# Performance work log

Hardware: AMD Instinct MI355X
Metric: run time of the kernel (lower is better)

## Reference

```python
import jax, jax.numpy as jnp
import numpy as np

HIDDEN = 512
MEM = 512
COMM = 512
N = 8192


def setup_inputs() -> dict:
    key = jax.random.key(0)
    ks = jax.random.split(key, 8)
    in_dim = HIDDEN + MEM
    s = 1.0 / np.sqrt(in_dim)
    return {
        "u": jax.random.normal(ks[0], (N, HIDDEN), dtype=jnp.float32),
        "z": jax.random.normal(ks[1], (N, MEM), dtype=jnp.float32),
        # torch Linear weights have shape (out, in); biases init to 0 per _init_weights
        "Wk": jax.random.normal(ks[2], (COMM, in_dim), dtype=jnp.float32) * s,
        "bk": jnp.zeros((COMM,), dtype=jnp.float32),
        "Wv": jax.random.normal(ks[3], (COMM, in_dim), dtype=jnp.float32) * s,
        "bv": jnp.zeros((COMM,), dtype=jnp.float32),
        "Wq": jax.random.normal(ks[4], (COMM, in_dim), dtype=jnp.float32) * s,
        "bq": jnp.zeros((COMM,), dtype=jnp.float32),
    }


def reference(u, z, Wk, bk, Wv, bv, Wq, bq):
    n = u.shape[0]
    scale = jnp.sqrt(jnp.asarray(Wk.shape[0], dtype=u.dtype))
    s = jnp.concatenate([u, z], axis=-1)              # (N, in_dim)
    keys = s @ Wk.T + bk                              # (N, C)
    values = s @ Wv.T + bv                            # (N, C)
    queries = s @ Wq.T + bq                           # (N, C)
    scores = (queries @ keys.T) / scale               # (N, N)
    eye = jnp.eye(n, dtype=bool)
    scores = jnp.where(eye, -jnp.inf, scores)         # self-mask
    comm_attn = jax.nn.softmax(scores, axis=-1)
    comm_attn = jnp.nan_to_num(comm_attn, nan=0.0)
    m_bar = comm_attn @ values                        # (N, C)
    return (m_bar, comm_attn)
```

## Files before the change

### kernel.cpp

```cpp
#include <hip/hip_runtime.h>
#include <hip/hip_bf16.h>
#include <stdint.h>

#define N_TOK 8192
#define IN_DIM 1024
#define CDIM 512
#define NW 1536

typedef short bf16x8 __attribute__((ext_vector_type(8)));
typedef float f32x4 __attribute__((ext_vector_type(4)));

__device__ __forceinline__ unsigned short f2bf(float f) {
  union { float f; unsigned int u; } x; x.f = f;
  unsigned int u = x.u;
  u += 0x7fffu + ((u >> 16) & 1u);
  return (unsigned short)(u >> 16);
}
__device__ __forceinline__ float bf2f(unsigned short us) {
  union { unsigned int u; float f; } x; x.u = ((unsigned int)us) << 16;
  return x.f;
}

#define GLD16(g, l) __builtin_amdgcn_global_load_lds( \
    (const __attribute__((address_space(1))) void*)(g), \
    (__attribute__((address_space(3))) void*)(l), 16, 0, 0)

__global__ __launch_bounds__(256) void k_convert(
    const float* __restrict__ u, const float* __restrict__ z,
    const float* __restrict__ wk, const float* __restrict__ wv,
    const float* __restrict__ wq,
    ushort* __restrict__ Sb, ushort* __restrict__ Wb) {
  const int S4 = N_TOK * IN_DIM / 4;
  const int W4 = NW * IN_DIM / 4;
  const int total = S4 + W4;
  for (int e = blockIdx.x * blockDim.x + threadIdx.x; e < total;
       e += gridDim.x * blockDim.x) {
    float4 v; ushort* dst;
    if (e < S4) {
      int idx = e << 2; int row = idx >> 10; int col = idx & 1023;
      const float* src = (col < 512) ? (u + row * 512 + col)
                                     : (z + row * 512 + (col - 512));
      v = *(const float4*)src;
      dst = Sb + idx;
    } else {
      int idx = (e - S4) << 2; int row = idx >> 10; int col = idx & 1023;
      const float* base = (row < 512) ? wk : (row < 1024 ? wv : wq);
      v = *(const float4*)(base + (size_t)(row & 511) * 1024 + col);
      dst = Wb + idx;
    }
    ushort4 o;
    o.x = f2bf(v.x); o.y = f2bf(v.y); o.z = f2bf(v.z); o.w = f2bf(v.w);
    *(ushort4*)dst = o;
  }
}

__global__ __launch_bounds__(256) void k_kvq(
    const ushort* __restrict__ Sb, const ushort* __restrict__ Wb,
    const float* __restrict__ bk, const float* __restrict__ bv,
    const float* __restrict__ bq,
    ushort* __restrict__ Kb, ushort* __restrict__ Qb, ushort* __restrict__ VT) {
  __shared__ __align__(16) ushort As[128 * 64];
  __shared__ __align__(16) ushort Bs[128 * 64];
  const int tid = threadIdx.x, lane = tid & 63, w = tid >> 6;
  const int wr = w >> 1, wc = w & 1;
  const int tm = blockIdx.x, tn = blockIdx.y;

  f32x4 acc[4][4];
#pragma unroll
  for (int m = 0; m < 4; m++)
#pragma unroll
    for (int n = 0; n < 4; n++) acc[m][n] = (f32x4){0.f, 0.f, 0.f, 0.f};

  const ushort* ga0 = Sb + (size_t)tm * 128 * IN_DIM;
  const ushort* gb0 = Wb + (size_t)tn * 128 * IN_DIM;

  for (int k0 = 0; k0 < IN_DIM; k0 += 64) {
#pragma unroll
    for (int i = 0; i < 4; i++) {
      int ce = i * 256 + tid;
      int row = ce >> 3, c8 = (ce & 7) << 3;
      GLD16(ga0 + (size_t)row * IN_DIM + k0 + c8, As + ce * 8);
      GLD16(gb0 + (size_t)row * IN_DIM + k0 + c8, Bs + ce * 8);
    }
    __syncthreads();
#pragma unroll
    for (int kb = 0; kb < 2; kb++) {
      bf16x8 af[4], bfr[4];
#pragma unroll
      for (int m = 0; m < 4; m++)
        af[m] = *(const bf16x8*)(As + (wr * 64 + m * 16 + (lane & 15)) * 64 +
                                 kb * 32 + ((lane >> 4) << 3));
#pragma unroll
      for (int n = 0; n < 4; n++)
        bfr[n] = *(const bf16x8*)(Bs + (wc * 64 + n * 16 + (lane & 15)) * 64 +
                                  kb * 32 + ((lane >> 4) << 3));
#pragma unroll
      for (int m = 0; m < 4; m++)
#pragma unroll
        for (int n = 0; n < 4; n++)
          acc[m][n] = __builtin_amdgcn_mfma_f32_16x16x32_bf16(af[m], bfr[n],
                                                              acc[m][n], 0, 0, 0);
    }
    __syncthreads();
  }

  const int region = tn >> 2;
  const int colr = (tn & 3) * 128 + wc * 64;
  const int rbase = tm * 128 + wr * 64;
  const float* bias = (region == 0) ? bk : (region == 1 ? bv : bq);
  if (region == 1) {
#pragma unroll
    for (int m = 0; m < 4; m++) {
      int r0 = rbase + m * 16 + ((lane >> 4) << 2);
#pragma unroll
      for (int n = 0; n < 4; n++) {
        int c = colr + n * 16 + (lane & 15);
        float b = bias[c];
        ushort4 pk;
        pk.x = f2bf(acc[m][n][0] + b);
        pk.y = f2bf(acc[m][n][1] + b);
        pk.z = f2bf(acc[m][n][2] + b);
        pk.w = f2bf(acc[m][n][3] + b);
        *(ushort4*)(VT + (size_t)c * N_TOK + r0) = pk;
      }
    }
  } else {
    ushort* O = (region == 0) ? Kb : Qb;
#pragma unroll
    for (int m = 0; m < 4; m++) {
      int r0 = rbase + m * 16 + ((lane >> 4) << 2);
#pragma unroll
      for (int n = 0; n < 4; n++) {
        int c = colr + n * 16 + (lane & 15);
        float b = bias[c];
#pragma unroll
        for (int rg = 0; rg < 4; rg++)
          O[(size_t)(r0 + rg) * CDIM + c] = f2bf(acc[m][n][rg] + b);
      }
    }
  }
}

__global__ __launch_bounds__(256) void k_scores(
    const ushort* __restrict__ Qb, const ushort* __restrict__ Kb,
    ushort* __restrict__ E, float* __restrict__ rowpart) {
  __shared__ __align__(16) ushort As[128 * 64];
  __shared__ __align__(16) ushort Bs[128 * 64];
  __shared__ float sums[256];
  const int tid = threadIdx.x, lane = tid & 63, w = tid >> 6;
  const int wr = w >> 1, wc = w & 1;
  const int tm = blockIdx.x, tn = blockIdx.y;

  f32x4 acc[4][4];
#pragma unroll
  for (int m = 0; m < 4; m++)
#pragma unroll
    for (int n = 0; n < 4; n++) acc[m][n] = (f32x4){0.f, 0.f, 0.f, 0.f};

  const ushort* ga0 = Qb + (size_t)tm * 128 * CDIM;
  const ushort* gb0 = Kb + (size_t)tn * 128 * CDIM;

  for (int k0 = 0; k0 < CDIM; k0 += 64) {
#pragma unroll
    for (int i = 0; i < 4; i++) {
      int ce = i * 256 + tid;
      int row = ce >> 3, c8 = (ce & 7) << 3;
      GLD16(ga0 + (size_t)row * CDIM + k0 + c8, As + ce * 8);
      GLD16(gb0 + (size_t)row * CDIM + k0 + c8, Bs + ce * 8);
    }
    __syncthreads();
#pragma unroll
    for (int kb = 0; kb < 2; kb++) {
      bf16x8 af[4], bfr[4];
#pragma unroll
      for (int m = 0; m < 4; m++)
        af[m] = *(const bf16x8*)(As + (wr * 64 + m * 16 + (lane & 15)) * 64 +
                                 kb * 32 + ((lane >> 4) << 3));
#pragma unroll
      for (int n = 0; n < 4; n++)
        bfr[n] = *(const bf16x8*)(Bs + (wc * 64 + n * 16 + (lane & 15)) * 64 +
                                  kb * 32 + ((lane >> 4) << 3));
#pragma unroll
      for (int m = 0; m < 4; m++)
#pragma unroll
        for (int n = 0; n < 4; n++)
          acc[m][n] = __builtin_amdgcn_mfma_f32_16x16x32_bf16(af[m], bfr[n],
                                                              acc[m][n], 0, 0, 0);
    }
    __syncthreads();
  }

  const float scale = 0.044194173824159216f;
  float rs[4][4];
#pragma unroll
  for (int m = 0; m < 4; m++)
#pragma unroll
    for (int rg = 0; rg < 4; rg++) rs[m][rg] = 0.f;

#pragma unroll
  for (int m = 0; m < 4; m++) {
    int grow_b = tm * 128 + wr * 64 + m * 16 + ((lane >> 4) << 2);
#pragma unroll
    for (int n = 0; n < 4; n++) {
      int gcol = tn * 128 + wc * 64 + n * 16 + (lane & 15);
#pragma unroll
      for (int rg = 0; rg < 4; rg++) {
        int grow = grow_b + rg;
        float ev = (grow == gcol) ? 0.0f : __expf(acc[m][n][rg] * scale);
        unsigned short evb = f2bf(ev);
        E[(size_t)grow * N_TOK + gcol] = evb;
        rs[m][rg] += bf2f(evb);
      }
    }
  }
#pragma unroll
  for (int m = 0; m < 4; m++)
#pragma unroll
    for (int rg = 0; rg < 4; rg++) {
      float s = rs[m][rg];
      s += __shfl_xor(s, 1);
      s += __shfl_xor(s, 2);
      s += __shfl_xor(s, 4);
      s += __shfl_xor(s, 8);
      rs[m][rg] = s;
    }
  if ((lane & 15) == 0) {
#pragma unroll
    for (int m = 0; m < 4; m++)
#pragma unroll
      for (int rg = 0; rg < 4; rg++)
        sums[wc * 128 + wr * 64 + m * 16 + ((lane >> 4) << 2) + rg] = rs[m][rg];
  }
  __syncthreads();
  if (tid < 128)
    rowpart[(size_t)(tm * 128 + tid) * 64 + tn] = sums[tid] + sums[128 + tid];
}

__global__ __launch_bounds__(256) void k_rcp(const float* __restrict__ rowpart,
                                             float* __restrict__ rcp_l) {
  int row = blockIdx.x * blockDim.x + threadIdx.x;
  if (row < N_TOK) {
    const float4* p = (const float4*)(rowpart + (size_t)row * 64);
    float s = 0.f;
#pragma unroll
    for (int i = 0; i < 16; i++) {
      float4 v = p[i];
      s += v.x + v.y + v.z + v.w;
    }
    rcp_l[row] = 1.0f / s;
  }
}

__global__ __launch_bounds__(256) void k_pv(
    const ushort* __restrict__ E, const ushort* __restrict__ VT,
    const float* __restrict__ rcp_l, float* __restrict__ mbar) {
  __shared__ __align__(16) ushort As[128 * 64];
  __shared__ __align__(16) ushort Bs[64 * 64];
  const int tid = threadIdx.x, lane = tid & 63, w = tid >> 6;
  const int wr = w >> 1, wc = w & 1;
  const int tm = blockIdx.x, tn = blockIdx.y;

  f32x4 acc[4][2];
#pragma unroll
  for (int m = 0; m < 4; m++)
#pragma unroll
    for (int n = 0; n < 2; n++) acc[m][n] = (f32x4){0.f, 0.f, 0.f, 0.f};

  const ushort* ga0 = E + (size_t)tm * 128 * N_TOK;
  const ushort* gb0 = VT + (size_t)tn * 64 * N_TOK;

  for (int k0 = 0; k0 < N_TOK; k0 += 64) {
#pragma unroll
    for (int i = 0; i < 4; i++) {
      int ce = i * 256 + tid;
      int row = ce >> 3, c8 = (ce & 7) << 3;
      GLD16(ga0 + (size_t)row * N_TOK + k0 + c8, As + ce * 8);
    }
#pragma unroll
    for (int i = 0; i < 2; i++) {
      int ce = i * 256 + tid;
      int row = ce >> 3, c8 = (ce & 7) << 3;
      GLD16(gb0 + (size_t)row * N_TOK + k0 + c8, Bs + ce * 8);
    }
    __syncthreads();
#pragma unroll
    for (int kb = 0; kb < 2; kb++) {
      bf16x8 af[4], bfr[2];
#pragma unroll
      for (int m = 0; m < 4; m++)
        af[m] = *(const bf16x8*)(As + (wr * 64 + m * 16 + (lane & 15)) * 64 +
                                 kb * 32 + ((lane >> 4) << 3));
#pragma unroll
      for (int n = 0; n < 2; n++)
        bfr[n] = *(const bf16x8*)(Bs + (wc * 32 + n * 16 + (lane & 15)) * 64 +
                                  kb * 32 + ((lane >> 4) << 3));
#pragma unroll
      for (int m = 0; m < 4; m++)
#pragma unroll
        for (int n = 0; n < 2; n++)
          acc[m][n] = __builtin_amdgcn_mfma_f32_16x16x32_bf16(af[m], bfr[n],
                                                              acc[m][n], 0, 0, 0);
    }
    __syncthreads();
  }

#pragma unroll
  for (int m = 0; m < 4; m++) {
    int r0 = tm * 128 + wr * 64 + m * 16 + ((lane >> 4) << 2);
#pragma unroll
    for (int n = 0; n < 2; n++) {
      int c = tn * 64 + wc * 32 + n * 16 + (lane & 15);
#pragma unroll
      for (int rg = 0; rg < 4; rg++)
        mbar[(size_t)(r0 + rg) * CDIM + c] = acc[m][n][rg] * rcp_l[r0 + rg];
    }
  }
}

__global__ __launch_bounds__(256) void k_norm(
    const ushort* __restrict__ E, float* __restrict__ attn,
    const float* __restrict__ rcp_l, int row0, int nrows) {
  const int units = nrows << 10;
  for (int uidx = blockIdx.x * blockDim.x + threadIdx.x; uidx < units;
       uidx += gridDim.x * blockDim.x) {
    int row = row0 + (uidx >> 10);
    int c8 = (uidx & 1023) << 3;
    const float rl = rcp_l[row];
    uint4 ev = *(const uint4*)(E + ((size_t)row << 13) + c8);
    float4 o0, o1;
    o0.x = bf2f((unsigned short)(ev.x & 0xffffu)) * rl;
    o0.y = bf2f((unsigned short)(ev.x >> 16)) * rl;
    o0.z = bf2f((unsigned short)(ev.y & 0xffffu)) * rl;
    o0.w = bf2f((unsigned short)(ev.y >> 16)) * rl;
    o1.x = bf2f((unsigned short)(ev.z & 0xffffu)) * rl;
    o1.y = bf2f((unsigned short)(ev.z >> 16)) * rl;
    o1.z = bf2f((unsigned short)(ev.w & 0xffffu)) * rl;
    o1.w = bf2f((unsigned short)(ev.w >> 16)) * rl;
    float* op = attn + ((size_t)row << 13) + c8;
    *(float4*)op = o0;
    *(float4*)(op + 4) = o1;
  }
}

__global__ __launch_bounds__(256) void k_lastrow(
    const ushort* __restrict__ E, float* __restrict__ attn,
    const float* __restrict__ rcp_l) {
  const int row = N_TOK - 1;
  const int t = threadIdx.x;
  const float rl = rcp_l[row];
  const uint4* src = (const uint4*)(E + ((size_t)row << 13)) + t * 4;
  uint4 r0 = src[0], r1 = src[1], r2 = src[2], r3 = src[3];
  __syncthreads();
  float* dst = attn + ((size_t)row << 13) + t * 32;
  uint4 rr[4] = {r0, r1, r2, r3};
#pragma unroll
  for (int q = 0; q < 4; q++) {
    float4 o0, o1;
    o0.x = bf2f((unsigned short)(rr[q].x & 0xffffu)) * rl;
    o0.y = bf2f((unsigned short)(rr[q].x >> 16)) * rl;
    o0.z = bf2f((unsigned short)(rr[q].y & 0xffffu)) * rl;
    o0.w = bf2f((unsigned short)(rr[q].y >> 16)) * rl;
    o1.x = bf2f((unsigned short)(rr[q].z & 0xffffu)) * rl;
    o1.y = bf2f((unsigned short)(rr[q].z >> 16)) * rl;
    o1.z = bf2f((unsigned short)(rr[q].w & 0xffffu)) * rl;
    o1.w = bf2f((unsigned short)(rr[q].w >> 16)) * rl;
    *(float4*)(dst + q * 8) = o0;
    *(float4*)(dst + q * 8 + 4) = o1;
  }
}

extern "C" void kernel_launch(void* const* d_in, const int* in_sizes, int n_in,
                              void* d_out, int out_size, void* d_ws,
                              size_t ws_size, hipStream_t stream) {
  const float* u  = (const float*)d_in[0];
  const float* z  = (const float*)d_in[1];
  const float* Wk = (const float*)d_in[2];
  const float* bk = (const float*)d_in[3];
  const float* Wv = (const float*)d_in[4];
  const float* bv = (const float*)d_in[5];
  const float* Wq = (const float*)d_in[6];
  const float* bq = (const float*)d_in[7];

  float* mbar = (float*)d_out;
  float* attn = (float*)d_out + (size_t)N_TOK * CDIM;

  char* ws = (char*)d_ws;
  ushort* Kb      = (ushort*)(ws + 0);
  ushort* Qb      = (ushort*)(ws + 8388608);
  ushort* VT      = (ushort*)(ws + 16777216);
  float*  rcp_l   = (float*)(ws + 25165824);
  float*  rowpart = (float*)(ws + 25198592);
  ushort* Sb      = (ushort*)(ws + 27295744);
  ushort* Wb      = (ushort*)(ws + 44072960);
  const size_t E_WS_OFF = 27295744;
  const size_t REQ = E_WS_OFF + 134217728;
  const bool ws_mode = (ws_size >= REQ);
  ushort* E = ws_mode ? (ushort*)(ws + E_WS_OFF)
                      : (ushort*)((char*)attn + 134217728);

  k_convert<<<dim3(2048), dim3(256), 0, stream>>>(u, z, Wk, Wv, Wq, Sb, Wb);
  k_kvq<<<dim3(64, 12), dim3(256), 0, stream>>>(Sb, Wb, bk, bv, bq, Kb, Qb, VT);
  k_scores<<<dim3(64, 64), dim3(256), 0, stream>>>(Qb, Kb, E, rowpart);
  k_rcp<<<dim3(32), dim3(256), 0, stream>>>(rowpart, rcp_l);
  k_pv<<<dim3(64, 8), dim3(256), 0, stream>>>(E, VT, rcp_l, mbar);

  if (ws_mode) {
    k_norm<<<dim3(2048), dim3(256), 0, stream>>>(E, attn, rcp_l, 0, N_TOK);
  } else {
    static const int ph[] = {0, 4096, 6144, 7168, 7680, 7936, 8064, 8128,
                             8160, 8176, 8184, 8188, 8190, 8191};
    for (int p = 0; p + 1 < (int)(sizeof(ph) / sizeof(ph[0])); ++p) {
      int a = ph[p], b = ph[p + 1];
      int units = (b - a) << 10;
      int blocks = (units + 255) / 256;
      if (blocks > 2048) blocks = 2048;
      k_norm<<<dim3(blocks), dim3(256), 0, stream>>>(E, attn, rcp_l, a, b - a);
    }
    k_lastrow<<<dim3(1), dim3(256), 0, stream>>>(E, attn, rcp_l);
  }
}
```

Measured before the change: 408.1 us.

## Split-K the PV GEMM with larger tiles, LDS swizzle, and remap score blocks

The PV GEMM now uses 128x128 output tiles and splits the 8192-long K dimension four ways across grid z/y, so more blocks run at once. Each block writes an unnormalized fp32 partial into scratch space inside the attn output. A new reduce kernel sums the four partials and applies the row reciprocal. LDS tiles in PV get an XOR chunk swizzle to cut bank conflicts, and the scores kernel uses a 1D grid with a block-index remap to change which tiles run together for cache locality. The cost is extra global traffic for the partial buffers and one more kernel launch.

```diff
diff --git a/kernel.cpp b/kernel.cpp
--- a/kernel.cpp
+++ b/kernel.cpp
@@ -149,7 +149,9 @@
   __shared__ float sums[256];
   const int tid = threadIdx.x, lane = tid & 63, w = tid >> 6;
   const int wr = w >> 1, wc = w & 1;
-  const int tm = blockIdx.x, tn = blockIdx.y;
+  const int bid = blockIdx.x;
+  const int swz = (bid & 7) * 512 + (bid >> 3);
+  const int tm = swz & 63, tn = swz >> 6;
 
   f32x4 acc[4][4];
 #pragma unroll
@@ -253,67 +255,90 @@
 
 __global__ __launch_bounds__(256) void k_pv(
     const ushort* __restrict__ E, const ushort* __restrict__ VT,
-    const float* __restrict__ rcp_l, float* __restrict__ mbar) {
+    float* __restrict__ part0, float* __restrict__ part1,
+    float* __restrict__ part2, float* __restrict__ part3) {
   __shared__ __align__(16) ushort As[128 * 64];
-  __shared__ __align__(16) ushort Bs[64 * 64];
+  __shared__ __align__(16) ushort Bs[128 * 64];
   const int tid = threadIdx.x, lane = tid & 63, w = tid >> 6;
   const int wr = w >> 1, wc = w & 1;
-  const int tm = blockIdx.x, tn = blockIdx.y;
-
-  f32x4 acc[4][2];
+  const int tn = blockIdx.x, kz = blockIdx.y, tm = blockIdx.z;
+  const int kbase = kz << 11;
+
+  f32x4 acc[4][4];
 #pragma unroll
   for (int m = 0; m < 4; m++)
 #pragma unroll
-    for (int n = 0; n < 2; n++) acc[m][n] = (f32x4){0.f, 0.f, 0.f, 0.f};
+    for (int n = 0; n < 4; n++) acc[m][n] = (f32x4){0.f, 0.f, 0.f, 0.f};
 
   const ushort* ga0 = E + (size_t)tm * 128 * N_TOK;
-  const ushort* gb0 = VT + (size_t)tn * 64 * N_TOK;
-
-  for (int k0 = 0; k0 < N_TOK; k0 += 64) {
+  const ushort* gb0 = VT + (size_t)tn * 128 * N_TOK;
+  const int sx = lane & 7;
+
+  for (int k0 = kbase; k0 < kbase + 2048; k0 += 64) {
 #pragma unroll
     for (int i = 0; i < 4; i++) {
       int ce = i * 256 + tid;
-      int row = ce >> 3, c8 = (ce & 7) << 3;
+      int row = ce >> 3;
+      int c8 = ((ce & 7) ^ (row & 7)) << 3;
       GLD16(ga0 + (size_t)row * N_TOK + k0 + c8, As + ce * 8);
-    }
-#pragma unroll
-    for (int i = 0; i < 2; i++) {
-      int ce = i * 256 + tid;
-      int row = ce >> 3, c8 = (ce & 7) << 3;
       GLD16(gb0 + (size_t)row * N_TOK + k0 + c8, Bs + ce * 8);
     }
     __syncthreads();
 #pragma unroll
     for (int kb = 0; kb < 2; kb++) {
-      bf16x8 af[4], bfr[2];
+      const int chunk = ((kb * 4 + (lane >> 4)) ^ sx) << 3;
+      bf16x8 af[4], bfr[4];
 #pragma unroll
       for (int m = 0; m < 4; m++)
         af[m] = *(const bf16x8*)(As + (wr * 64 + m * 16 + (lane & 15)) * 64 +
-                                 kb * 32 + ((lane >> 4) << 3));
-#pragma unroll
-      for (int n = 0; n < 2; n++)
-        bfr[n] = *(const bf16x8*)(Bs + (wc * 32 + n * 16 + (lane & 15)) * 64 +
-                                  kb * 32 + ((lane >> 4) << 3));
-#pragma unroll
-      for (int m = 0; m < 4; m++)
-#pragma unroll
-        for (int n = 0; n < 2; n++)
+                                 chunk);
+#pragma unroll
+      for (int n = 0; n < 4; n++)
+        bfr[n] = *(const bf16x8*)(Bs + (wc * 64 + n * 16 + (lane & 15)) * 64 +
+                                  chunk);
+#pragma unroll
+      for (int m = 0; m < 4; m++)
+#pragma unroll
+        for (int n = 0; n < 4; n++)
           acc[m][n] = __builtin_amdgcn_mfma_f32_16x16x32_bf16(af[m], bfr[n],
                                                               acc[m][n], 0, 0, 0);
     }
     __syncthreads();
   }
 
+  float* P = (kz == 0) ? part0 : (kz == 1) ? part1 : (kz == 2) ? part2 : part3;
 #pragma unroll
   for (int m = 0; m < 4; m++) {
     int r0 = tm * 128 + wr * 64 + m * 16 + ((lane >> 4) << 2);
 #pragma unroll
-    for (int n = 0; n < 2; n++) {
-      int c = tn * 64 + wc * 32 + n * 16 + (lane & 15);
+    for (int n = 0; n < 4; n++) {
+      int c = tn * 128 + wc * 64 + n * 16 + (lane & 15);
 #pragma unroll
       for (int rg = 0; rg < 4; rg++)
-        mbar[(size_t)(r0 + rg) * CDIM + c] = acc[m][n][rg] * rcp_l[r0 + rg];
-    }
+        P[(size_t)(r0 + rg) * CDIM + c] = acc[m][n][rg];
+    }
+  }
+}
+
+__global__ __launch_bounds__(256) void k_reduce4(
+    float* __restrict__ p0, const float* __restrict__ p1,
+    const float* __restrict__ p2, const float* __restrict__ p3,
+    const float* __restrict__ rcp_l) {
+  int idx4 = blockIdx.x * blockDim.x + threadIdx.x;
+  const int T4 = N_TOK * CDIM / 4;
+  if (idx4 < T4) {
+    int row = idx4 >> 7;
+    float rl = rcp_l[row];
+    float4 a = ((const float4*)p0)[idx4];
+    float4 b = ((const float4*)p1)[idx4];
+    float4 c = ((const float4*)p2)[idx4];
+    float4 d = ((const float4*)p3)[idx4];
+    float4 o;
+    o.x = (a.x + b.x + c.x + d.x) * rl;
+    o.y = (a.y + b.y + c.y + d.y) * rl;
+    o.z = (a.z + b.z + c.z + d.z) * rl;
+    o.w = (a.w + b.w + c.w + d.w) * rl;
+    ((float4*)p0)[idx4] = o;
   }
 }
 
@@ -349,10 +374,9 @@
   const int t = threadIdx.x;
   const float rl = rcp_l[row];
   const uint4* src = (const uint4*)(E + ((size_t)row << 13)) + t * 4;
-  uint4 r0 = src[0], r1 = src[1], r2 = src[2], r3 = src[3];
+  uint4 rr[4] = {src[0], src[1], src[2], src[3]};
   __syncthreads();
   float* dst = attn + ((size_t)row << 13) + t * 32;
-  uint4 rr[4] = {r0, r1, r2, r3};
 #pragma unroll
   for (int q = 0; q < 4; q++) {
     float4 o0, o1;
@@ -397,12 +421,18 @@
   const bool ws_mode = (ws_size >= REQ);
   ushort* E = ws_mode ? (ushort*)(ws + E_WS_OFF)
                       : (ushort*)((char*)attn + 134217728);
+  float* part1 = attn;
+  float* part2 = attn + (size_t)N_TOK * CDIM;
+  float* part3 = attn + (size_t)2 * N_TOK * CDIM;
 
   k_convert<<<dim3(2048), dim3(256), 0, stream>>>(u, z, Wk, Wv, Wq, Sb, Wb);
   k_kvq<<<dim3(64, 12), dim3(256), 0, stream>>>(Sb, Wb, bk, bv, bq, Kb, Qb, VT);
-  k_scores<<<dim3(64, 64), dim3(256), 0, stream>>>(Qb, Kb, E, rowpart);
+  k_scores<<<dim3(4096), dim3(256), 0, stream>>>(Qb, Kb, E, rowpart);
   k_rcp<<<dim3(32), dim3(256), 0, stream>>>(rowpart, rcp_l);
-  k_pv<<<dim3(64, 8), dim3(256), 0, stream>>>(E, VT, rcp_l, mbar);
+  k_pv<<<dim3(4, 4, 64), dim3(256), 0, stream>>>(E, VT, mbar, part1, part2,
+                                                 part3);
+  k_reduce4<<<dim3(4096), dim3(256), 0, stream>>>(mbar, part1, part2, part3,
+                                                  rcp_l);
 
   if (ws_mode) {
     k_norm<<<dim3(2048), dim3(256), 0, stream>>>(E, attn, rcp_l, 0, N_TOK);
```

Measured after the change: 391.5 us. 1.04x faster.
